# Performance work log

Measured on AMD Instinct MI355X. Metric: run time of the kernel, lower is better.

The kernel has to match this reference:

```python
import jax, jax.numpy as jnp
import numpy as np

N_NODES = 100000
N_EDGES = 1600000

def setup_inputs() -> dict:
    key = jax.random.key(0)
    ks = jax.random.split(key, 6)
    x = jax.random.normal(ks[0], (N_NODES, 128), dtype=jnp.float32)
    edge_index = jax.random.randint(ks[1], (2, N_EDGES), 0, N_NODES, dtype=jnp.int64)
    edge_weight = jax.random.uniform(ks[2], (N_EDGES,), dtype=jnp.float32)
    # kaiming-uniform-like init for weights, zeros for biases (as in reset_parameters)
    bound1 = float(np.sqrt(6.0 / 128))
    W1 = jax.random.uniform(ks[3], (128, 128), minval=-bound1, maxval=bound1, dtype=jnp.float32)
    b1 = jnp.zeros((128,), dtype=jnp.float32)
    W2 = jax.random.uniform(ks[4], (128, 64), minval=-bound1, maxval=bound1, dtype=jnp.float32)
    b2 = jnp.zeros((64,), dtype=jnp.float32)
    return {"x": x, "edge_index": edge_index, "edge_weight": edge_weight,
            "W1": W1, "b1": b1, "W2": W2, "b2": b2}

def _gcn_conv(x, src, dst, ew, W, b):
    support = x @ W                      # [N, F_out] dense GEMM
    msgs = ew[:, None] * support[src]    # [E, F_out] gather + scale (spmm values)
    out = jax.ops.segment_sum(msgs, dst, num_segments=N_NODES)  # scatter-add
    return out + b

def reference(x, edge_index, edge_weight, W1, b1, W2, b2):
    dst, src = edge_index[0], edge_index[1]  # adj[dst, src] = edge_weight
    h = _gcn_conv(x, src, dst, edge_weight, W1, b1)
    h = jax.nn.relu(h)
    out = _gcn_conv(h, src, dst, edge_weight, W2, b2)
    return out
```

## Files before the change

### kernel.cpp

```cpp
#include <hip/hip_runtime.h>

#define N_NODES 100000
#define N_EDGES 1600000
#define NB 391
#define PAD 16
#define SC_EPB 2048
#define SC_BLOCKS ((N_EDGES + SC_EPB - 1) / SC_EPB)
#define LDA 136
#define NTILES ((N_NODES + 127) / 128)

#define XQ_SCALE (5.5f / 127.0f)
#define XQ_INV   (127.0f / 5.5f)

#define PREP_X_BLOCKS ((N_NODES * 32 + 255) / 256)
#define PREP_W_BLOCKS 48
#define PREP_H_BLOCKS NB

typedef unsigned int uint32;
typedef __attribute__((ext_vector_type(8))) short bf16x8;
typedef __attribute__((ext_vector_type(4))) float f32x4;

__device__ __forceinline__ uint32 bf16_rne(float f) {
    uint32 u = __float_as_uint(f);
    return (u + 0x7fffu + ((u >> 16) & 1u)) >> 16;
}
__device__ __forceinline__ uint32 pack_bf16x2(float lo, float hi) {
    return bf16_rne(lo) | (bf16_rne(hi) << 16);
}
__device__ __forceinline__ float bf16_lo(uint32 u) { return __uint_as_float(u << 16); }
__device__ __forceinline__ float bf16_hi(uint32 u) { return __uint_as_float(u & 0xFFFF0000u); }

__device__ __forceinline__ float ub0(uint32 u) { return (float)(u & 255u); }
__device__ __forceinline__ float ub1(uint32 u) { return (float)((u >> 8) & 255u); }
__device__ __forceinline__ float ub2(uint32 u) { return (float)((u >> 16) & 255u); }
__device__ __forceinline__ float ub3(uint32 u) { return (float)(u >> 24); }

__global__ __launch_bounds__(256) void prep(const float* __restrict__ x,
                                            const float* __restrict__ W1,
                                            const float* __restrict__ W2,
                                            const int* __restrict__ dst,
                                            uint32* __restrict__ xq,
                                            uint32* __restrict__ w1tb,
                                            uint32* __restrict__ w2tb,
                                            int* __restrict__ bktCnt) {
    const int b = blockIdx.x;
    if (b < PREP_X_BLOCKS) {
        const int t = b * 256 + threadIdx.x;
        if (t >= N_NODES * 32) return;
        const float4 v = ((const float4*)x)[t];
        const int q0 = (int)rintf(fminf(fmaxf(v.x * XQ_INV, -127.f), 127.f)) + 128;
        const int q1 = (int)rintf(fminf(fmaxf(v.y * XQ_INV, -127.f), 127.f)) + 128;
        const int q2 = (int)rintf(fminf(fmaxf(v.z * XQ_INV, -127.f), 127.f)) + 128;
        const int q3 = (int)rintf(fminf(fmaxf(v.w * XQ_INV, -127.f), 127.f)) + 128;
        xq[t] = (uint32)q0 | ((uint32)q1 << 8) | ((uint32)q2 << 16) | ((uint32)q3 << 24);
    } else if (b < PREP_X_BLOCKS + PREP_W_BLOCKS) {
        const int t = (b - PREP_X_BLOCKS) * 256 + threadIdx.x;
        if (t < 128 * 64) {
            const int n = t >> 6, kk = t & 63;
            w1tb[t] = pack_bf16x2(W1[(2 * kk) * 128 + n], W1[(2 * kk + 1) * 128 + n]);
        } else if (t < 128 * 64 + 64 * 64) {
            const int u = t - 128 * 64;
            const int n = u >> 6, kk = u & 63;
            w2tb[u] = pack_bf16x2(W2[(2 * kk) * 64 + n], W2[(2 * kk + 1) * 64 + n]);
        }
    } else {
        __shared__ int h[NB];
        const int bh = b - PREP_X_BLOCKS - PREP_W_BLOCKS;
        for (int i = threadIdx.x; i < NB; i += 256) h[i] = 0;
        __syncthreads();
        for (int e = bh * 256 + threadIdx.x; e < N_EDGES; e += NB * 256)
            atomicAdd(&h[dst[e] >> 8], 1);
        __syncthreads();
        for (int i = threadIdx.x; i < NB; i += 256)
            if (h[i]) atomicAdd(&bktCnt[i * PAD], h[i]);
    }
}

__global__ __launch_bounds__(512) void bucket_scan(const int* __restrict__ bktCnt,
                                                   int* __restrict__ bBase,
                                                   int* __restrict__ bCur,
                                                   int* __restrict__ offs) {
    __shared__ int s[512];
    const int t = threadIdx.x;
    int v = (t < NB) ? bktCnt[t * PAD] : 0;
    s[t] = v;
    __syncthreads();
#pragma unroll
    for (int off = 1; off < 512; off <<= 1) {
        int u = (t >= off) ? s[t - off] : 0;
        __syncthreads();
        s[t] += u;
        __syncthreads();
    }
    if (t < NB) {
        const int excl = s[t] - v;
        bBase[t] = excl;
        bCur[t * PAD] = excl;
    }
    if (t == 0) {
        bBase[NB] = N_EDGES;
        offs[N_NODES] = N_EDGES;
    }
}

__global__ __launch_bounds__(256) void bucket_scatter2(const int* __restrict__ dst,
                                                       const int* __restrict__ src,
                                                       const float* __restrict__ ew,
                                                       int* __restrict__ bCur,
                                                       int2* __restrict__ bucketed) {
    __shared__ int h[NB];
    __shared__ int cur[NB];
    const int base = blockIdx.x * SC_EPB;
    const int end  = min(base + SC_EPB, N_EDGES);

    for (int i = threadIdx.x; i < NB; i += 256) h[i] = 0;
    __syncthreads();
    for (int e = base + threadIdx.x; e < end; e += 256)
        atomicAdd(&h[dst[e] >> 8], 1);
    __syncthreads();
    for (int i = threadIdx.x; i < NB; i += 256) {
        const int c = h[i];
        cur[i] = c ? atomicAdd(&bCur[i * PAD], c) : 0;
    }
    __syncthreads();
    for (int e = base + threadIdx.x; e < end; e += 256) {
        const int d = dst[e];
        const int p = atomicAdd(&cur[d >> 8], 1);
        bucketed[p] = make_int2(src[e] | ((d & 255) << 17), __float_as_int(ew[e]));
    }
}

__global__ __launch_bounds__(256) void bucket_csr(const int2* __restrict__ bucketed,
                                                  const int* __restrict__ bBase,
                                                  int* __restrict__ offs,
                                                  int2* __restrict__ csr_ef) {
    __shared__ int sdeg[256];
    __shared__ int lcur[256];
    const int b   = blockIdx.x;
    const int t   = threadIdx.x;
    const int beg = bBase[b], end = bBase[b + 1];

    sdeg[t] = 0;
    __syncthreads();
    for (int j = beg + t; j < end; j += 256)
        atomicAdd(&sdeg[(bucketed[j].x >> 17) & 255], 1);
    __syncthreads();
    const int mydeg = sdeg[t];
#pragma unroll
    for (int off = 1; off < 256; off <<= 1) {
        int u = (t >= off) ? sdeg[t - off] : 0;
        __syncthreads();
        sdeg[t] += u;
        __syncthreads();
    }
    const int excl = sdeg[t] - mydeg;
    lcur[t] = excl;
    const int node = b * 256 + t;
    if (node < N_NODES) offs[node] = beg + excl;
    __syncthreads();

    for (int j = beg + t; j < end; j += 256) {
        const int2 v = bucketed[j];
        const int dl = (v.x >> 17) & 255;
        const int p  = beg + atomicAdd(&lcur[dl], 1);
        csr_ef[p] = make_int2(v.x & 0x1FFFF, v.y);
    }
}

template <int FEAT>
__global__ __launch_bounds__(256) void aggregate(const void* __restrict__ featv,
                                                 const int* __restrict__ offs,
                                                 const int2* __restrict__ csr_ef,
                                                 const float* __restrict__ bias,
                                                 void* __restrict__ outv) {
    const int n    = (blockIdx.x * 256 + threadIdx.x) >> 6;
    const int lane = threadIdx.x & 63;
    if (n >= N_NODES) return;
    const int beg = offs[n], end = offs[n + 1];
    const uint4* feat = (const uint4*)featv;

    if constexpr (FEAT == 128) {
        const int g = lane >> 3;
        const int f = lane & 7;

        float u0 = 0.f, u1 = 0.f, u2 = 0.f, u3 = 0.f;
        float u4 = 0.f, u5 = 0.f, u6 = 0.f, u7 = 0.f;
        float u8 = 0.f, u9 = 0.f, u10 = 0.f, u11 = 0.f;
        float u12 = 0.f, u13 = 0.f, u14 = 0.f, u15 = 0.f;
        float wsum = 0.f;

        for (int j = beg + g; j < end; j += 16) {
#pragma unroll
            for (int uu = 0; uu < 2; ++uu) {
                const int jj = j + uu * 8;
                if (uu == 0 || jj < end) {
                    const int2 e = csr_ef[jj];
                    const uint4 r = feat[(unsigned)(e.x * 8 + f)];
                    const float w = __int_as_float(e.y);
                    wsum += w;
                    u0  += w * ub0(r.x); u1  += w * ub1(r.x);
                    u2  += w * ub2(r.x); u3  += w * ub3(r.x);
                    u4  += w * ub0(r.y); u5  += w * ub1(r.y);
                    u6  += w * ub2(r.y); u7  += w * ub3(r.y);
                    u8  += w * ub0(r.z); u9  += w * ub1(r.z);
                    u10 += w * ub2(r.z); u11 += w * ub3(r.z);
                    u12 += w * ub0(r.w); u13 += w * ub1(r.w);
                    u14 += w * ub2(r.w); u15 += w * ub3(r.w);
                }
            }
        }

#pragma unroll
        for (int d = 8; d < 64; d <<= 1) {
            u0  += __shfl_xor(u0, d);  u1  += __shfl_xor(u1, d);
            u2  += __shfl_xor(u2, d);  u3  += __shfl_xor(u3, d);
            u4  += __shfl_xor(u4, d);  u5  += __shfl_xor(u5, d);
            u6  += __shfl_xor(u6, d);  u7  += __shfl_xor(u7, d);
            u8  += __shfl_xor(u8, d);  u9  += __shfl_xor(u9, d);
            u10 += __shfl_xor(u10, d); u11 += __shfl_xor(u11, d);
            u12 += __shfl_xor(u12, d); u13 += __shfl_xor(u13, d);
            u14 += __shfl_xor(u14, d); u15 += __shfl_xor(u15, d);
            wsum += __shfl_xor(wsum, d);
        }

        if (g == 0) {
            const float off128 = 128.f * wsum;
            const float s = XQ_SCALE;
            uint4 pA, pB;
            pA.x = pack_bf16x2(s * (u0 - off128),  s * (u1 - off128));
            pA.y = pack_bf16x2(s * (u2 - off128),  s * (u3 - off128));
            pA.z = pack_bf16x2(s * (u4 - off128),  s * (u5 - off128));
            pA.w = pack_bf16x2(s * (u6 - off128),  s * (u7 - off128));
            pB.x = pack_bf16x2(s * (u8 - off128),  s * (u9 - off128));
            pB.y = pack_bf16x2(s * (u10 - off128), s * (u11 - off128));
            pB.z = pack_bf16x2(s * (u12 - off128), s * (u13 - off128));
            pB.w = pack_bf16x2(s * (u14 - off128), s * (u15 - off128));
            ((uint4*)outv)[(size_t)n * 16 + f * 2]     = pA;
            ((uint4*)outv)[(size_t)n * 16 + f * 2 + 1] = pB;
        }
    } else {
        const int g  = lane >> 3;
        const int f4 = lane & 7;

        float a0 = 0.f, a1 = 0.f, a2 = 0.f, a3 = 0.f;
        float a4 = 0.f, a5 = 0.f, a6 = 0.f, a7 = 0.f;

        for (int j = beg + g; j < end; j += 16) {
            {
                const int2 e = csr_ef[j];
                const uint4 r = feat[(unsigned)(e.x * 8 + f4)];
                const float w = __int_as_float(e.y);
                a0 += w * bf16_lo(r.x); a1 += w * bf16_hi(r.x);
                a2 += w * bf16_lo(r.y); a3 += w * bf16_hi(r.y);
                a4 += w * bf16_lo(r.z); a5 += w * bf16_hi(r.z);
                a6 += w * bf16_lo(r.w); a7 += w * bf16_hi(r.w);
            }
            if (j + 8 < end) {
                const int2 e = csr_ef[j + 8];
                const uint4 r = feat[(unsigned)(e.x * 8 + f4)];
                const float w = __int_as_float(e.y);
                a0 += w * bf16_lo(r.x); a1 += w * bf16_hi(r.x);
                a2 += w * bf16_lo(r.y); a3 += w * bf16_hi(r.y);
                a4 += w * bf16_lo(r.z); a5 += w * bf16_hi(r.z);
                a6 += w * bf16_lo(r.w); a7 += w * bf16_hi(r.w);
            }
        }

#pragma unroll
        for (int d = 8; d < 64; d <<= 1) {
            a0 += __shfl_xor(a0, d); a1 += __shfl_xor(a1, d);
            a2 += __shfl_xor(a2, d); a3 += __shfl_xor(a3, d);
            a4 += __shfl_xor(a4, d); a5 += __shfl_xor(a5, d);
            a6 += __shfl_xor(a6, d); a7 += __shfl_xor(a7, d);
        }

        if (g == 0) {
            const float4* b4 = (const float4*)bias;
            const float4 bA = b4[f4 * 2];
            const float4 bB = b4[f4 * 2 + 1];
            float4 o0 = make_float4(a0 + bA.x, a1 + bA.y, a2 + bA.z, a3 + bA.w);
            float4 o1 = make_float4(a4 + bB.x, a5 + bB.y, a6 + bB.z, a7 + bB.w);
            ((float4*)outv)[(size_t)n * 16 + f4 * 2]     = o0;
            ((float4*)outv)[(size_t)n * 16 + f4 * 2 + 1] = o1;
        }
    }
}

__global__ __launch_bounds__(512) void gemm_fused(const uint32* __restrict__ aggPb,
                                                  const uint32* __restrict__ w1tb,
                                                  const float* __restrict__ b1,
                                                  const uint32* __restrict__ w2tb,
                                                  uint32* __restrict__ sup2b, int N) {
    __shared__ __align__(16) short As[128 * LDA];
    __shared__ __align__(16) short W1s[128 * LDA];
    __shared__ __align__(16) short W2s[64 * LDA];
    __shared__ __align__(16) short Ts[128 * LDA];

    const int tid = threadIdx.x;

    for (int i = tid; i < 128 * 16; i += 512)
        *(uint4*)&W1s[(i >> 4) * LDA + (i & 15) * 8] = ((const uint4*)w1tb)[i];
    for (int i = tid; i < 64 * 16; i += 512)
        *(uint4*)&W2s[(i >> 4) * LDA + (i & 15) * 8] = ((const uint4*)w2tb)[i];

    const int wave = tid >> 6;
    const int lane = tid & 63;
    const int m    = lane & 15;
    const int quad = lane >> 4;
    const int rowbase = (wave & 3) * 32;
    const int colbase = (wave >> 2) * 64;

    float b1r[4];
#pragma unroll
    for (int ct = 0; ct < 4; ++ct) b1r[ct] = b1[colbase + ct * 16 + m];

    for (int tile = blockIdx.x; tile < NTILES; tile += gridDim.x) {
        const int row0 = tile * 128;
        __syncthreads();

#pragma unroll
        for (int i = 0; i < 4; ++i) {
            const int idx = i * 512 + tid;
            const int row = idx >> 4, c4 = idx & 15;
            const int grow = row0 + row;
            uint4 v = make_uint4(0u, 0u, 0u, 0u);
            if (grow < N) v = ((const uint4*)aggPb)[(size_t)grow * 16 + c4];
            *(uint4*)&As[row * LDA + c4 * 8] = v;
        }
        __syncthreads();

        bf16x8 afrag[2][4];
#pragma unroll
        for (int ss = 0; ss < 2; ++ss)
#pragma unroll
            for (int ch = 0; ch < 4; ++ch)
                afrag[ss][ch] = *(const bf16x8*)&As[(rowbase + ss * 16 + m) * LDA + ch * 32 + quad * 8];

        f32x4 acc[2][4];
#pragma unroll
        for (int ss = 0; ss < 2; ++ss)
#pragma unroll
            for (int ct = 0; ct < 4; ++ct) acc[ss][ct] = (f32x4){0.f, 0.f, 0.f, 0.f};

#pragma unroll
        for (int ct = 0; ct < 4; ++ct) {
            bf16x8 bfr[4];
#pragma unroll
            for (int ch = 0; ch < 4; ++ch)
                bfr[ch] = *(const bf16x8*)&W1s[(colbase + ct * 16 + m) * LDA + ch * 32 + quad * 8];
#pragma unroll
            for (int ss = 0; ss < 2; ++ss)
#pragma unroll
                for (int ch = 0; ch < 4; ++ch)
                    acc[ss][ct] = __builtin_amdgcn_mfma_f32_16x16x32_bf16(
                        afrag[ss][ch], bfr[ch], acc[ss][ct], 0, 0, 0);
        }

#pragma unroll
        for (int ss = 0; ss < 2; ++ss)
#pragma unroll
            for (int ct = 0; ct < 4; ++ct)
#pragma unroll
                for (int r = 0; r < 4; ++r) {
                    const float v = fmaxf(acc[ss][ct][r] + b1r[ct], 0.f);
                    const int row = rowbase + ss * 16 + quad * 4 + r;
                    const int col = colbase + ct * 16 + m;
                    Ts[row * LDA + col] = (short)bf16_rne(v);
                }
        __syncthreads();

        const int rb2 = wave * 16;
        bf16x8 tfrag[4];
#pragma unroll
        for (int ch = 0; ch < 4; ++ch)
            tfrag[ch] = *(const bf16x8*)&Ts[(rb2 + m) * LDA + ch * 32 + quad * 8];

        f32x4 acc2[4];
#pragma unroll
        for (int ct = 0; ct < 4; ++ct) acc2[ct] = (f32x4){0.f, 0.f, 0.f, 0.f};
#pragma unroll
        for (int ct = 0; ct < 4; ++ct)
#pragma unroll
            for (int ch = 0; ch < 4; ++ch) {
                const bf16x8 bfr = *(const bf16x8*)&W2s[(ct * 16 + m) * LDA + ch * 32 + quad * 8];
                acc2[ct] = __builtin_amdgcn_mfma_f32_16x16x32_bf16(
                    tfrag[ch], bfr, acc2[ct], 0, 0, 0);
            }

#pragma unroll
        for (int ct = 0; ct < 4; ++ct)
#pragma unroll
            for (int r = 0; r < 4; ++r) {
                const int row = rb2 + quad * 4 + r;
                const int col = ct * 16 + m;
                As[row * LDA + col] = (short)bf16_rne(acc2[ct][r]);
            }
        __syncthreads();
#pragma unroll
        for (int i = 0; i < 2; ++i) {
            const int idx = i * 512 + tid;
            const int row = idx >> 3, c4 = idx & 7;
            if (row0 + row < N)
                ((uint4*)sup2b)[(size_t)(row0 + row) * 8 + c4] = *(uint4*)&As[row * LDA + c4 * 8];
        }
    }
}

extern "C" void kernel_launch(void* const* d_in, const int* in_sizes, int n_in,
                              void* d_out, int out_size, void* d_ws, size_t ws_size,
                              hipStream_t stream) {
    const float* x  = (const float*)d_in[0];
    const int*   ei = (const int*)d_in[1];
    const float* ew = (const float*)d_in[2];
    const float* W1 = (const float*)d_in[3];
    const float* b1 = (const float*)d_in[4];
    const float* W2 = (const float*)d_in[5];
    const float* b2 = (const float*)d_in[6];
    float* out = (float*)d_out;

    const int* dstIdx = ei;
    const int* srcIdx = ei + N_EDGES;

    uint32* xb      = (uint32*)d_ws;
    uint32* aggPb   = xb + (size_t)N_NODES * 64;
    uint32* w1tb    = aggPb + (size_t)N_NODES * 64;
    uint32* w2tb    = w1tb + 128 * 64;
    int2*   csr_ef  = (int2*)(xb + (size_t)N_NODES * 64 + (size_t)N_NODES * 128);
    int*    bktCnt  = (int*)(csr_ef + N_EDGES);
    int*    bCur    = bktCnt + NB * PAD;
    int*    bBase   = bCur + NB * PAD;
    int*    offs    = bBase + NB + 1;
    int2*   bucketed = (int2*)aggPb;
    uint32* sup2b   = xb;

    (void)hipMemsetAsync(bktCnt, 0, (size_t)NB * PAD * sizeof(int), stream);

    prep<<<PREP_X_BLOCKS + PREP_W_BLOCKS + PREP_H_BLOCKS, 256, 0, stream>>>(
        x, W1, W2, dstIdx, xb, w1tb, w2tb, bktCnt);

    bucket_scan<<<1, 512, 0, stream>>>(bktCnt, bBase, bCur, offs);
    bucket_scatter2<<<SC_BLOCKS, 256, 0, stream>>>(dstIdx, srcIdx, ew, bCur, bucketed);
    bucket_csr<<<NB, 256, 0, stream>>>(bucketed, bBase, offs, csr_ef);

    aggregate<128><<<(N_NODES * 64) / 256, 256, 0, stream>>>(xb, offs, csr_ef,
                                                             nullptr, aggPb);
    gemm_fused<<<256, 512, 0, stream>>>(aggPb, w1tb, b1, w2tb, sup2b, N_NODES);

    aggregate<64><<<(N_NODES * 64) / 256, 256, 0, stream>>>(sup2b, offs, csr_ef,
                                                            b2, out);
}
```

Measured before the change: 321.1 us.

## Fold bucket scan into scatter and CSR kernels, enlarge scatter blocks

Removes the separate single-block bucket_scan launch by having each scatter block redo the 391-entry prefix scan in shared memory, and each CSR block compute its bucket start by reducing the preceding counts. Scatter blocks now use 512 threads with 4096 edges per block, and the fused GEMM launch grows from 256 to 261 blocks. This saves one kernel launch and its serialisation, but every block repeats the scan and the CSR blocks do redundant global reads of the counts. bCur now starts at zero from the enlarged memset and holds only a relative offset.

Result: faster. 306.4 us (-4.6%).

```diff
diff --git a/kernel.cpp b/kernel.cpp
--- a/kernel.cpp
+++ b/kernel.cpp
@@ -4,10 +4,11 @@
 #define N_EDGES 1600000
 #define NB 391
 #define PAD 16
-#define SC_EPB 2048
+#define SC_EPB 4096
 #define SC_BLOCKS ((N_EDGES + SC_EPB - 1) / SC_EPB)
 #define LDA 136
 #define NTILES ((N_NODES + 127) / 128)
+#define GEMM_BLOCKS 261
 
 #define XQ_SCALE (5.5f / 127.0f)
 #define XQ_INV   (127.0f / 5.5f)
@@ -34,6 +35,10 @@
 __device__ __forceinline__ float ub1(uint32 u) { return (float)((u >> 8) & 255u); }
 __device__ __forceinline__ float ub2(uint32 u) { return (float)((u >> 16) & 255u); }
 __device__ __forceinline__ float ub3(uint32 u) { return (float)(u >> 24); }
+
+__device__ __forceinline__ uint32 q8(float v, float inv) {
+    return (uint32)((int)rintf(fminf(fmaxf(v * inv, -127.f), 127.f)) + 128);
+}
 
 __global__ __launch_bounds__(256) void prep(const float* __restrict__ x,
                                             const float* __restrict__ W1,
@@ -48,11 +53,8 @@
         const int t = b * 256 + threadIdx.x;
         if (t >= N_NODES * 32) return;
         const float4 v = ((const float4*)x)[t];
-        const int q0 = (int)rintf(fminf(fmaxf(v.x * XQ_INV, -127.f), 127.f)) + 128;
-        const int q1 = (int)rintf(fminf(fmaxf(v.y * XQ_INV, -127.f), 127.f)) + 128;
-        const int q2 = (int)rintf(fminf(fmaxf(v.z * XQ_INV, -127.f), 127.f)) + 128;
-        const int q3 = (int)rintf(fminf(fmaxf(v.w * XQ_INV, -127.f), 127.f)) + 128;
-        xq[t] = (uint32)q0 | ((uint32)q1 << 8) | ((uint32)q2 << 16) | ((uint32)q3 << 24);
+        xq[t] = q8(v.x, XQ_INV) | (q8(v.y, XQ_INV) << 8)
+              | (q8(v.z, XQ_INV) << 16) | (q8(v.w, XQ_INV) << 24);
     } else if (b < PREP_X_BLOCKS + PREP_W_BLOCKS) {
         const int t = (b - PREP_X_BLOCKS) * 256 + threadIdx.x;
         if (t < 128 * 64) {
@@ -76,54 +78,41 @@
     }
 }
 
-__global__ __launch_bounds__(512) void bucket_scan(const int* __restrict__ bktCnt,
-                                                   int* __restrict__ bBase,
-                                                   int* __restrict__ bCur,
-                                                   int* __restrict__ offs) {
-    __shared__ int s[512];
-    const int t = threadIdx.x;
-    int v = (t < NB) ? bktCnt[t * PAD] : 0;
-    s[t] = v;
-    __syncthreads();
-#pragma unroll
-    for (int off = 1; off < 512; off <<= 1) {
-        int u = (t >= off) ? s[t - off] : 0;
-        __syncthreads();
-        s[t] += u;
-        __syncthreads();
-    }
-    if (t < NB) {
-        const int excl = s[t] - v;
-        bBase[t] = excl;
-        bCur[t * PAD] = excl;
-    }
-    if (t == 0) {
-        bBase[NB] = N_EDGES;
-        offs[N_NODES] = N_EDGES;
-    }
-}
-
-__global__ __launch_bounds__(256) void bucket_scatter2(const int* __restrict__ dst,
+__global__ __launch_bounds__(512) void bucket_scatter2(const int* __restrict__ dst,
                                                        const int* __restrict__ src,
                                                        const float* __restrict__ ew,
+                                                       const int* __restrict__ bktCnt,
                                                        int* __restrict__ bCur,
                                                        int2* __restrict__ bucketed) {
     __shared__ int h[NB];
     __shared__ int cur[NB];
+    __shared__ int s[512];
+    const int t    = threadIdx.x;
     const int base = blockIdx.x * SC_EPB;
     const int end  = min(base + SC_EPB, N_EDGES);
 
-    for (int i = threadIdx.x; i < NB; i += 256) h[i] = 0;
-    __syncthreads();
-    for (int e = base + threadIdx.x; e < end; e += 256)
+    for (int i = t; i < NB; i += 512) h[i] = 0;
+    __syncthreads();
+    for (int e = base + t; e < end; e += 512)
         atomicAdd(&h[dst[e] >> 8], 1);
     __syncthreads();
-    for (int i = threadIdx.x; i < NB; i += 256) {
-        const int c = h[i];
-        cur[i] = c ? atomicAdd(&bCur[i * PAD], c) : 0;
-    }
-    __syncthreads();
-    for (int e = base + threadIdx.x; e < end; e += 256) {
+
+    const int v = (t < NB) ? bktCnt[t * PAD] : 0;
+    s[t] = v;
+    __syncthreads();
+#pragma unroll
+    for (int off = 1; off < 512; off <<= 1) {
+        const int u = (t >= off) ? s[t - off] : 0;
+        __syncthreads();
+        s[t] += u;
+        __syncthreads();
+    }
+    if (t < NB) {
+        const int c = h[t];
+        cur[t] = (s[t] - v) + (c ? atomicAdd(&bCur[t * PAD], c) : 0);
+    }
+    __syncthreads();
+    for (int e = base + t; e < end; e += 512) {
         const int d = dst[e];
         const int p = atomicAdd(&cur[d >> 8], 1);
         bucketed[p] = make_int2(src[e] | ((d & 255) << 17), __float_as_int(ew[e]));
@@ -131,14 +120,32 @@
 }
 
 __global__ __launch_bounds__(256) void bucket_csr(const int2* __restrict__ bucketed,
-                                                  const int* __restrict__ bBase,
+                                                  const int* __restrict__ bktCnt,
                                                   int* __restrict__ offs,
                                                   int2* __restrict__ csr_ef) {
     __shared__ int sdeg[256];
     __shared__ int lcur[256];
-    const int b   = blockIdx.x;
-    const int t   = threadIdx.x;
-    const int beg = bBase[b], end = bBase[b + 1];
+    __shared__ int red[256];
+    __shared__ int s_beg, s_end;
+    const int b = blockIdx.x;
+    const int t = threadIdx.x;
+
+    int partial = 0;
+    for (int k = t; k < b; k += 256) partial += bktCnt[k * PAD];
+    red[t] = partial;
+    __syncthreads();
+#pragma unroll
+    for (int off = 128; off > 0; off >>= 1) {
+        if (t < off) red[t] += red[t + off];
+        __syncthreads();
+    }
+    if (t == 0) {
+        s_beg = red[0];
+        s_end = red[0] + bktCnt[b * PAD];
+        if (b == 0) offs[N_NODES] = N_EDGES;
+    }
+    __syncthreads();
+    const int beg = s_beg, end = s_end;
 
     sdeg[t] = 0;
     __syncthreads();
@@ -425,26 +432,25 @@
     uint32* aggPb   = xb + (size_t)N_NODES * 64;
     uint32* w1tb    = aggPb + (size_t)N_NODES * 64;
     uint32* w2tb    = w1tb + 128 * 64;
-    int2*   csr_ef  = (int2*)(xb + (size_t)N_NODES * 64 + (size_t)N_NODES * 128);
+    int2*   csr_ef  = (int2*)(xb + (size_t)N_NODES * 192);
     int*    bktCnt  = (int*)(csr_ef + N_EDGES);
     int*    bCur    = bktCnt + NB * PAD;
-    int*    bBase   = bCur + NB * PAD;
-    int*    offs    = bBase + NB + 1;
+    int*    offs    = bCur + NB * PAD;
     int2*   bucketed = (int2*)aggPb;
     uint32* sup2b   = xb;
 
-    (void)hipMemsetAsync(bktCnt, 0, (size_t)NB * PAD * sizeof(int), stream);
+    (void)hipMemsetAsync(bktCnt, 0, (size_t)2 * NB * PAD * sizeof(int), stream);
 
     prep<<<PREP_X_BLOCKS + PREP_W_BLOCKS + PREP_H_BLOCKS, 256, 0, stream>>>(
         x, W1, W2, dstIdx, xb, w1tb, w2tb, bktCnt);
 
-    bucket_scan<<<1, 512, 0, stream>>>(bktCnt, bBase, bCur, offs);
-    bucket_scatter2<<<SC_BLOCKS, 256, 0, stream>>>(dstIdx, srcIdx, ew, bCur, bucketed);
-    bucket_csr<<<NB, 256, 0, stream>>>(bucketed, bBase, offs, csr_ef);
+    bucket_scatter2<<<SC_BLOCKS, 512, 0, stream>>>(dstIdx, srcIdx, ew, bktCnt,
+                                                   bCur, bucketed);
+    bucket_csr<<<NB, 256, 0, stream>>>(bucketed, bktCnt, offs, csr_ef);
 
     aggregate<128><<<(N_NODES * 64) / 256, 256, 0, stream>>>(xb, offs, csr_ef,
                                                              nullptr, aggPb);
-    gemm_fused<<<256, 512, 0, stream>>>(aggPb, w1tb, b1, w2tb, sup2b, N_NODES);
+    gemm_fused<<<GEMM_BLOCKS, 512, 0, stream>>>(aggPb, w1tb, b1, w2tb, sup2b, N_NODES);
 
     aggregate<64><<<(N_NODES * 64) / 256, 256, 0, stream>>>(sup2b, offs, csr_ef,
                                                             b2, out);
```
